# Optimization experiments

Hardware: AMD Instinct MI355X
Metric: run time of the kernel (lower is better)

## Reference

```python
import jax, jax.numpy as jnp
from jax import lax
import numpy as np

H = 64
NS = 20000
NR = 2000
T = 24
ALPHA = 0.5


def _p(key, *shape):
    return jax.random.normal(key, shape, dtype=jnp.float32) * 0.05


def setup_inputs() -> dict:
    key = jax.random.key(0)
    ks = jax.random.split(key, 40)
    inp = {
        "x_store": jax.random.normal(ks[0], (NS, T), dtype=jnp.float32),
        "x_region": jax.random.normal(ks[1], (NR, T), dtype=jnp.float32),
        "edge_ss": jax.random.randint(ks[2], (2, 640000), 0, NS),
        "edge_rs_src": jax.random.randint(ks[3], (160000,), 0, NR),
        "edge_rs_dst": jax.random.randint(ks[4], (160000,), 0, NS),
        "edge_sr_src": jax.random.randint(ks[5], (160000,), 0, NS),
        "edge_sr_dst": jax.random.randint(ks[6], (160000,), 0, NR),
        # LSTM pretransform params (torch gate order i,f,g,o)
        "Wih_s": _p(ks[7], 4 * H, 1), "Whh_s": _p(ks[8], 4 * H, H),
        "bih_s": _p(ks[9], 4 * H), "bhh_s": _p(ks[10], 4 * H),
        "Wih_r": _p(ks[11], 4 * H, 1), "Whh_r": _p(ks[12], 4 * H, H),
        "bih_r": _p(ks[13], 4 * H), "bhh_r": _p(ks[14], 4 * H),
        # DirSageConv (store-store)
        "W_s2d": _p(ks[15], H, H), "b_s2d": _p(ks[16], H),
        "W_d2s": _p(ks[17], H, H), "b_d2s": _p(ks[18], H),
        "W_self": _p(ks[19], H, H), "b_self": _p(ks[20], H),
        # SAGEConv region->store (lin_l w/ bias, lin_r no bias)
        "Wl_rs": _p(ks[21], H, H), "bl_rs": _p(ks[22], H), "Wr_rs": _p(ks[23], H, H),
        # SAGEConv store->region
        "Wl_sr": _p(ks[24], H, H), "bl_sr": _p(ks[25], H), "Wr_sr": _p(ks[26], H, H),
        # final linear
        "Wf": _p(ks[27], H, H), "bf": _p(ks[28], H),
    }
    return inp


def lstm_last(x, Wih, Whh, bih, bhh):
    # x: [N, T] scalar sequences (input_size=1). Returns last hidden state [N, H].
    N = x.shape[0]
    w_in = Wih[:, 0]  # [4H]
    b = bih + bhh

    def step(carry, xt):
        h, c = carry
        gates = xt[:, None] * w_in[None, :] + h @ Whh.T + b  # [N, 4H]
        i, f, g, o = jnp.split(gates, 4, axis=1)
        c = jax.nn.sigmoid(f) * c + jax.nn.sigmoid(i) * jnp.tanh(g)
        h = jax.nn.sigmoid(o) * jnp.tanh(c)
        return (h, c), None

    z = jnp.zeros((N, Whh.shape[1]), x.dtype)
    (h, _), _ = lax.scan(step, (z, z), x.T)
    return h


def mean_aggr(feats, dst_idx, num_dst):
    # mean of gathered edge messages per destination node (0 for isolated nodes)
    s = jax.ops.segment_sum(feats, dst_idx, num_segments=num_dst)
    cnt = jax.ops.segment_sum(jnp.ones(dst_idx.shape, feats.dtype), dst_idx, num_segments=num_dst)
    return s / jnp.maximum(cnt, 1.0)[:, None]


def reference(x_store, x_region, edge_ss, edge_rs_src, edge_rs_dst,
              edge_sr_src, edge_sr_dst,
              Wih_s, Whh_s, bih_s, bhh_s, Wih_r, Whh_r, bih_r, bhh_r,
              W_s2d, b_s2d, W_d2s, b_d2s, W_self, b_self,
              Wl_rs, bl_rs, Wr_rs, Wl_sr, bl_sr, Wr_sr, Wf, bf):
    # per-node-type LSTM pretransform -> [N, H]
    hs = lstm_last(x_store, Wih_s, Whh_s, bih_s, bhh_s)
    hr = lstm_last(x_region, Wih_r, Whh_r, bih_r, bhh_r)

    # DirSageConv on (store, link, store)
    src, dst = edge_ss[0], edge_ss[1]
    a_fwd = mean_aggr(hs[src], dst, NS) @ W_s2d.T + b_s2d   # src -> dst
    a_rev = mean_aggr(hs[dst], src, NS) @ W_d2s.T + b_d2s   # dst -> src
    dir_out = hs @ W_self.T + b_self + (1.0 - ALPHA) * a_fwd + ALPHA * a_rev

    # SAGEConv (region, influences, store)
    rs_out = mean_aggr(hr[edge_rs_src], edge_rs_dst, NS) @ Wl_rs.T + bl_rs + hs @ Wr_rs.T

    # SAGEConv (store, rev_influences, region)
    sr_out = mean_aggr(hs[edge_sr_src], edge_sr_dst, NR) @ Wl_sr.T + bl_sr + hr @ Wr_sr.T

    # HeteroConv aggr='mean' over edge types per dst node type
    store_h = (dir_out + rs_out) * 0.5
    region_h = sr_out

    # residual + relu
    store_h = jax.nn.relu(store_h + hs)
    region_h = jax.nn.relu(region_h + hr)  # computed as in torch, unused by output

    return store_h @ Wf.T + bf
```

## Files before the change

kernel.cpp:

```cpp
#include <hip/hip_runtime.h>
#include <hip/hip_bf16.h>

#define TT 24
#define NSTORE 20000
#define NREGION 2000
#define NE_SS 640000
#define NE_RS 160000
#define BN 32
#define SUBS 96
#define NGRP 8
#define CAPF 80
#define CAPS 32
#define POISON ((int)0xAAAAAAAAu)

typedef __attribute__((ext_vector_type(8))) short bf16x8;
typedef __attribute__((ext_vector_type(4))) float f32x4;

__device__ __forceinline__ float rcpf(float x) { return __builtin_amdgcn_rcpf(x); }
__device__ __forceinline__ float sigm(float x) { return rcpf(1.0f + __expf(-x)); }
__device__ __forceinline__ float tanh_(float x) { return fmaf(-2.0f, rcpf(1.0f + __expf(2.0f * x)), 1.0f); }

__device__ __forceinline__ short f2bs(float x) {
    __hip_bfloat16 h = __float2bfloat16(x);
    return *reinterpret_cast<short*>(&h);
}
__device__ __forceinline__ bf16x8 pack8(float4 a, float4 b) {
    bf16x8 r;
    r[0] = f2bs(a.x); r[1] = f2bs(a.y); r[2] = f2bs(a.z); r[3] = f2bs(a.w);
    r[4] = f2bs(b.x); r[5] = f2bs(b.y); r[6] = f2bs(b.z); r[7] = f2bs(b.w);
    return r;
}
__device__ __forceinline__ unsigned packbf2(float lo, float hi) {
    return ((unsigned)(unsigned short)f2bs(hi) << 16) | (unsigned)(unsigned short)f2bs(lo);
}
__device__ __forceinline__ float bf_lo(unsigned u) { return __uint_as_float(u << 16); }
__device__ __forceinline__ float bf_hi(unsigned u) { return __uint_as_float(u & 0xffff0000u); }

__device__ __forceinline__ f32x4 mfma16(bf16x8 a, bf16x8 b, f32x4 c) {
    return __builtin_amdgcn_mfma_f32_16x16x32_bf16(a, b, c, 0, 0, 0);
}

__global__ __launch_bounds__(256)
void lstm_fill(const float* __restrict__ xs, const float* __restrict__ WihS,
               const float* __restrict__ WhhS, const float* __restrict__ bihS,
               const float* __restrict__ bhhS,
               const float* __restrict__ xr, const float* __restrict__ WihR,
               const float* __restrict__ WhhR, const float* __restrict__ bihR,
               const float* __restrict__ bhhR,
               unsigned* __restrict__ hsOut, unsigned* __restrict__ hrOut,
               const int* __restrict__ ss_src, const int* __restrict__ ss_dst,
               const int* __restrict__ rs_src, const int* __restrict__ rs_dst,
               int* __restrict__ curF, int* __restrict__ curR, int* __restrict__ curS,
               int* __restrict__ eidF, int* __restrict__ eidR, int* __restrict__ eidS,
               int nBlocksStore, int nBlocksLstm)
{
    const int tid = threadIdx.x;

    if ((int)blockIdx.x >= nBlocksLstm) {
        const int fb = (int)blockIdx.x - nBlocksLstm;
        const int g = fb & (NGRP - 1);
        const int sub = fb / NGRP;
        const int lo = g * (NSTORE / NGRP), hi = lo + NSTORE / NGRP;
        const int stride = SUBS * 256;

        for (int t = sub * 256 + tid; t < NE_SS / 4; t += stride) {
            const int4 s4 = ((const int4*)ss_src)[t];
            const int4 d4 = ((const int4*)ss_dst)[t];
            const int ss[4] = {s4.x, s4.y, s4.z, s4.w};
            const int dd[4] = {d4.x, d4.y, d4.z, d4.w};
            #pragma unroll
            for (int e = 0; e < 4; ++e) {
                if (dd[e] >= lo && dd[e] < hi) {
                    int p = atomicAdd(&curF[dd[e]], 1) - POISON;
                    if (p < CAPF) eidF[dd[e] * CAPF + p] = ss[e];
                }
                if (ss[e] >= lo && ss[e] < hi) {
                    int p = atomicAdd(&curR[ss[e]], 1) - POISON;
                    if (p < CAPF) eidR[ss[e] * CAPF + p] = dd[e];
                }
            }
        }
        for (int t = sub * 256 + tid; t < NE_RS / 4; t += stride) {
            const int4 s4 = ((const int4*)rs_src)[t];
            const int4 d4 = ((const int4*)rs_dst)[t];
            const int ss[4] = {s4.x, s4.y, s4.z, s4.w};
            const int dd[4] = {d4.x, d4.y, d4.z, d4.w};
            #pragma unroll
            for (int e = 0; e < 4; ++e) {
                if (dd[e] >= lo && dd[e] < hi) {
                    int p = atomicAdd(&curS[dd[e]], 1) - POISON;
                    if (p < CAPS) eidS[dd[e] * CAPS + p] = ss[e];
                }
            }
        }
        return;
    }

    __shared__ unsigned hbU[2][32][36];
    __shared__ float xbuf[BN][25];

    const float *x, *Wih, *Whh, *bih, *bhh;
    unsigned* hout; int N, node0;
    if ((int)blockIdx.x < nBlocksStore) {
        x = xs; Wih = WihS; Whh = WhhS; bih = bihS; bhh = bhhS;
        hout = hsOut; N = NSTORE; node0 = blockIdx.x * BN;
    } else {
        x = xr; Wih = WihR; Whh = WhhR; bih = bihR; bhh = bhhR;
        hout = hrOut; N = NREGION; node0 = ((int)blockIdx.x - nBlocksStore) * BN;
    }

    const int w = tid >> 6, lane = tid & 63;
    const int l15 = lane & 15, q = lane >> 4;

    for (int i = tid; i < BN * TT; i += 256) {
        int n = i / TT, t = i - n * TT;
        int gn = node0 + n;
        xbuf[n][t] = (gn < N) ? x[gn * TT + t] : 0.0f;
    }

    bf16x8 Bf[4][2];
    #pragma unroll
    for (int g = 0; g < 4; ++g)
        #pragma unroll
        for (int kt = 0; kt < 2; ++kt) {
            const float* wrow = Whh + (g * 64 + (w << 4) + l15) * 64 + q * 8 + kt * 32;
            float4 v0 = *(const float4*)wrow;
            float4 v1 = *(const float4*)(wrow + 4);
            Bf[g][kt] = pack8(v0, v1);
        }

    float win[4], bsum[4];
    #pragma unroll
    for (int g = 0; g < 4; ++g) {
        int gi = g * 64 + (w << 4) + l15;
        win[g]  = Wih[gi];
        bsum[g] = bih[gi] + bhh[gi];
    }

    __syncthreads();

    float cc[2][4], hv[2][4];
    #pragma unroll
    for (int m = 0; m < 2; ++m)
        #pragma unroll
        for (int r = 0; r < 4; ++r) cc[m][r] = 0.0f;

    for (int t = 0; t < TT; ++t) {
        const int cur = t & 1, prev = cur ^ 1;

        bf16x8 Af[2][2];
        if (t > 0) {
            #pragma unroll
            for (int m = 0; m < 2; ++m)
                #pragma unroll
                for (int kt = 0; kt < 2; ++kt)
                    Af[m][kt] = *(const bf16x8*)&hbU[prev][l15 + 16 * m][(q << 2) + (kt << 4)];
        }

        f32x4 acc[4][2];
        float xv[2][4];
        #pragma unroll
        for (int m = 0; m < 2; ++m)
            #pragma unroll
            for (int r = 0; r < 4; ++r) xv[m][r] = xbuf[16 * m + q * 4 + r][t];
        #pragma unroll
        for (int g = 0; g < 4; ++g)
            #pragma unroll
            for (int m = 0; m < 2; ++m)
                #pragma unroll
                for (int r = 0; r < 4; ++r)
                    acc[g][m][r] = fmaf(xv[m][r], win[g], bsum[g]);

        if (t > 0) {
            #pragma unroll
            for (int g = 0; g < 4; ++g)
                #pragma unroll
                for (int m = 0; m < 2; ++m) {
                    acc[g][m] = mfma16(Af[m][0], Bf[g][0], acc[g][m]);
                    acc[g][m] = mfma16(Af[m][1], Bf[g][1], acc[g][m]);
                }
        }

        #pragma unroll
        for (int m = 0; m < 2; ++m)
            #pragma unroll
            for (int r = 0; r < 4; ++r) {
                float ig = sigm(acc[0][m][r]);
                float fg = sigm(acc[1][m][r]);
                float gg = tanh_(acc[2][m][r]);
                float og = sigm(acc[3][m][r]);
                float cn = fmaf(fg, cc[m][r], ig * gg);
                cc[m][r] = cn;
                hv[m][r] = og * tanh_(cn);
            }

        #pragma unroll
        for (int m = 0; m < 2; ++m)
            #pragma unroll
            for (int r = 0; r < 4; ++r) {
                float other = __shfl_xor(hv[m][r], 1);
                if ((l15 & 1) == 0)
                    hbU[cur][16 * m + 4 * q + r][(w << 3) + (l15 >> 1)] = packbf2(hv[m][r], other);
            }
        __syncthreads();
    }

    for (int i = tid; i < 32 * 32; i += 256) {
        int n = i >> 5, kp = i & 31;
        int gn = node0 + n;
        if (gn < N) hout[gn * 32 + kp] = hbU[1][n][kp];
    }
}

__global__ __launch_bounds__(256)
void gather_means(const unsigned* __restrict__ hsU, const unsigned* __restrict__ hrU,
                  const int* __restrict__ curF, const int* __restrict__ curR,
                  const int* __restrict__ curS,
                  const int* __restrict__ eidF, const int* __restrict__ eidR,
                  const int* __restrict__ eidS,
                  unsigned* __restrict__ xcatU)
{
    const int id = blockIdx.x * 4 + (threadIdx.x >> 6);
    const int lane = threadIdx.x & 63;
    const int sec = id / NSTORE;
    const int n   = id - sec * NSTORE;
    const int o8 = lane >> 3, l7 = lane & 7;

    unsigned* row = xcatU + (size_t)n * 128;

    if (sec == 0 && lane < 32) row[lane] = hsU[n * 32 + lane];

    const unsigned* feat = (sec == 2) ? hrU : hsU;
    const int* seg; int cnt, cap;
    if (sec == 0)      { seg = eidF + n * CAPF; cnt = curF[n] - POISON; cap = CAPF; }
    else if (sec == 1) { seg = eidR + n * CAPF; cnt = curR[n] - POISON; cap = CAPF; }
    else               { seg = eidS + n * CAPS; cnt = curS[n] - POISON; cap = CAPS; }
    int e = cnt < cap ? cnt : cap;

    float a[8];
    #pragma unroll
    for (int k = 0; k < 8; ++k) a[k] = 0.0f;

    for (int i = 0; i < e; i += 16) {
        int i0 = i + o8;
        if (i0 < e) {
            uint4 u = *(const uint4*)&feat[seg[i0] * 32 + 4 * l7];
            a[0] += bf_lo(u.x); a[1] += bf_hi(u.x);
            a[2] += bf_lo(u.y); a[3] += bf_hi(u.y);
            a[4] += bf_lo(u.z); a[5] += bf_hi(u.z);
            a[6] += bf_lo(u.w); a[7] += bf_hi(u.w);
        }
        int i1 = i + 8 + o8;
        if (i1 < e) {
            uint4 u = *(const uint4*)&feat[seg[i1] * 32 + 4 * l7];
            a[0] += bf_lo(u.x); a[1] += bf_hi(u.x);
            a[2] += bf_lo(u.y); a[3] += bf_hi(u.y);
            a[4] += bf_lo(u.z); a[5] += bf_hi(u.z);
            a[6] += bf_lo(u.w); a[7] += bf_hi(u.w);
        }
    }
    #pragma unroll
    for (int k = 0; k < 8; ++k) {
        a[k] += __shfl_xor(a[k], 8);
        a[k] += __shfl_xor(a[k], 16);
        a[k] += __shfl_xor(a[k], 32);
    }
    float c = rcpf(fmaxf((float)cnt, 1.0f));
    if (lane < 8) {
        uint4 o;
        o.x = packbf2(a[0] * c, a[1] * c);
        o.y = packbf2(a[2] * c, a[3] * c);
        o.z = packbf2(a[4] * c, a[5] * c);
        o.w = packbf2(a[6] * c, a[7] * c);
        *(uint4*)&row[(sec + 1) * 32 + 4 * l7] = o;
    }
}

__global__ __launch_bounds__(256, 2)
void combine_mm(const unsigned* __restrict__ xcatU,
                const float* __restrict__ Ws2d, const float* __restrict__ bs2d,
                const float* __restrict__ Wd2s, const float* __restrict__ bd2s,
                const float* __restrict__ Wself, const float* __restrict__ bself,
                const float* __restrict__ Wlrs, const float* __restrict__ blrs,
                const float* __restrict__ Wrrs,
                const float* __restrict__ Wfm, const float* __restrict__ bfv,
                float* __restrict__ out)
{
    __shared__ float Xs[64][68];
    __shared__ float Ps[64][64];
    __shared__ float Us[64][68];
    __shared__ float Wfs[64][68];
    __shared__ float biasc[64];

    const int tid = threadIdx.x;
    const int node0 = blockIdx.x * 64;

    for (int i = tid; i < 4096; i += 256) {
        int jp = i >> 6, j = i & 63;
        Wfs[j][jp] = Wfm[i];
    }
    if (tid < 64)
        biasc[tid] = bself[tid] + 0.5f * bs2d[tid] + 0.5f * bd2s[tid] + blrs[tid];

    const int jg = tid & 15, ng = tid >> 4;
    const int j0 = jg * 4, n0 = ng * 4;

    float acc[4][4];
    #pragma unroll
    for (int dn = 0; dn < 4; ++dn)
        #pragma unroll
        for (int dj = 0; dj < 4; ++dj) acc[dn][dj] = 0.0f;

    const int sj = tid >> 2, skb = tid & 3;

    for (int ci = 0; ci < 4; ++ci) {
        const int c = (ci + 1) & 3;
        __syncthreads();

        {
            int n = tid >> 2;
            int gn = node0 + n; if (gn > NSTORE - 1) gn = NSTORE - 1;
            const unsigned* src = xcatU + (size_t)gn * 128 + c * 32 + (tid & 3) * 8;
            uint4 u0 = *(const uint4*)src;
            uint4 u1 = *(const uint4*)(src + 4);
            unsigned uu[8] = {u0.x, u0.y, u0.z, u0.w, u1.x, u1.y, u1.z, u1.w};
            int k0 = (tid & 3) * 16;
            #pragma unroll
            for (int e = 0; e < 8; ++e) {
                Xs[k0 + 2 * e][n]     = bf_lo(uu[e]);
                Xs[k0 + 2 * e + 1][n] = bf_hi(uu[e]);
            }
        }
        {
            const float* W1; float scale;
            if (c == 0)      { W1 = Wself; scale = 1.0f; }
            else if (c == 1) { W1 = Ws2d;  scale = 0.5f; }
            else if (c == 2) { W1 = Wd2s;  scale = 0.5f; }
            else             { W1 = Wlrs;  scale = 1.0f; }
            #pragma unroll
            for (int qq = 0; qq < 4; ++qq) {
                int k0 = skb * 16 + qq * 4;
                float4 v = *(const float4*)(W1 + sj * 64 + k0);
                if (c == 0) {
                    float4 v2 = *(const float4*)(Wrrs + sj * 64 + k0);
                    v.x += v2.x; v.y += v2.y; v.z += v2.z; v.w += v2.w;
                } else {
                    v.x *= scale; v.y *= scale; v.z *= scale; v.w *= scale;
                }
                Ps[k0][sj] = v.x; Ps[k0 + 1][sj] = v.y;
                Ps[k0 + 2][sj] = v.z; Ps[k0 + 3][sj] = v.w;
            }
        }
        __syncthreads();

        #pragma unroll 4
        for (int k = 0; k < 64; ++k) {
            float4 wv = *(const float4*)&Ps[k][j0];
            float4 xv = *(const float4*)&Xs[k][n0];
            float x4[4] = {xv.x, xv.y, xv.z, xv.w};
            float w4[4] = {wv.x, wv.y, wv.z, wv.w};
            #pragma unroll
            for (int dn = 0; dn < 4; ++dn)
                #pragma unroll
                for (int dj = 0; dj < 4; ++dj)
                    acc[dn][dj] = fmaf(x4[dn], w4[dj], acc[dn][dj]);
        }
    }

    #pragma unroll
    for (int dn = 0; dn < 4; ++dn)
        #pragma unroll
        for (int dj = 0; dj < 4; ++dj) {
            float h = Xs[j0 + dj][n0 + dn];
            float u = fmaxf(fmaf(0.5f, acc[dn][dj] + biasc[j0 + dj], h), 0.0f);
            Us[j0 + dj][n0 + dn] = u;
        }
    __syncthreads();

    float o[4][4];
    #pragma unroll
    for (int dn = 0; dn < 4; ++dn)
        #pragma unroll
        for (int dj = 0; dj < 4; ++dj) o[dn][dj] = 0.0f;

    #pragma unroll 4
    for (int k = 0; k < 64; ++k) {
        float4 wv = *(const float4*)&Wfs[k][j0];
        float4 uv = *(const float4*)&Us[k][n0];
        float u4[4] = {uv.x, uv.y, uv.z, uv.w};
        float w4[4] = {wv.x, wv.y, wv.z, wv.w};
        #pragma unroll
        for (int dn = 0; dn < 4; ++dn)
            #pragma unroll
            for (int dj = 0; dj < 4; ++dj)
                o[dn][dj] = fmaf(u4[dn], w4[dj], o[dn][dj]);
    }

    float4 bfe = *(const float4*)(bfv + j0);
    #pragma unroll
    for (int dn = 0; dn < 4; ++dn) {
        int gn = node0 + n0 + dn;
        if (gn < NSTORE) {
            float4 v = make_float4(o[dn][0] + bfe.x, o[dn][1] + bfe.y,
                                   o[dn][2] + bfe.z, o[dn][3] + bfe.w);
            *(float4*)&out[gn * 64 + j0] = v;
        }
    }
}

extern "C" void kernel_launch(void* const* d_in, const int* in_sizes, int n_in,
                              void* d_out, int out_size, void* d_ws, size_t ws_size,
                              hipStream_t stream)
{
    const float* xs     = (const float*)d_in[0];
    const float* xr     = (const float*)d_in[1];
    const int*   e_ss   = (const int*)d_in[2];
    const int*   rs_src = (const int*)d_in[3];
    const int*   rs_dst = (const int*)d_in[4];
    const float* WihS = (const float*)d_in[7];
    const float* WhhS = (const float*)d_in[8];
    const float* bihS = (const float*)d_in[9];
    const float* bhhS = (const float*)d_in[10];
    const float* WihR = (const float*)d_in[11];
    const float* WhhR = (const float*)d_in[12];
    const float* bihR = (const float*)d_in[13];
    const float* bhhR = (const float*)d_in[14];
    const float* Ws2d = (const float*)d_in[15];
    const float* bs2d = (const float*)d_in[16];
    const float* Wd2s = (const float*)d_in[17];
    const float* bd2s = (const float*)d_in[18];
    const float* Wself = (const float*)d_in[19];
    const float* bself = (const float*)d_in[20];
    const float* Wlrs = (const float*)d_in[21];
    const float* blrs = (const float*)d_in[22];
    const float* Wrrs = (const float*)d_in[23];
    const float* Wfm = (const float*)d_in[27];
    const float* bfv = (const float*)d_in[28];

    const int* ss_src = e_ss;
    const int* ss_dst = e_ss + NE_SS;

    unsigned* hsU   = (unsigned*)d_ws;
    unsigned* hrU   = hsU + 640000;
    unsigned* xcatU = hrU + 64000;
    int*      ib    = (int*)(xcatU + 2560000);
    int* curF = ib;
    int* curR = ib + 20000;
    int* curS = ib + 40000;
    int* eidF = ib + 60000;
    int* eidR = eidF + NSTORE * CAPF;
    int* eidS = eidR + NSTORE * CAPF;

    const int storeBlocks  = (NSTORE + BN - 1) / BN;
    const int regionBlocks = (NREGION + BN - 1) / BN;
    const int lstmBlocks   = storeBlocks + regionBlocks;
    const int fillBlocks   = NGRP * SUBS;

    lstm_fill<<<lstmBlocks + fillBlocks, 256, 0, stream>>>(
        xs, WihS, WhhS, bihS, bhhS, xr, WihR, WhhR, bihR, bhhR,
        hsU, hrU, ss_src, ss_dst, rs_src, rs_dst,
        curF, curR, curS, eidF, eidR, eidS,
        storeBlocks, lstmBlocks);

    gather_means<<<3 * NSTORE / 4, 256, 0, stream>>>(hsU, hrU,
                                                     curF, curR, curS,
                                                     eidF, eidR, eidS, xcatU);

    combine_mm<<<(NSTORE + 63) / 64, 256, 0, stream>>>(xcatU,
                                                       Ws2d, bs2d, Wd2s, bd2s,
                                                       Wself, bself, Wlrs, blrs, Wrrs,
                                                       Wfm, bfv, (float*)d_out);
}
```

Baseline: 274.8 us.

## Split fused LSTM/edge-bucketing kernel into separate sequential launches

Breaks the combined kernel, where LSTM blocks and edge-bucketing blocks ran side by side in one grid, into two launches: an edge fill kernel followed by an LSTM-only kernel. Each kernel gets its own register and occupancy profile, so the fill work is no longer constrained by the LSTM kernel's resource use. The cost is that the two phases no longer overlap on the GPU and there is an extra launch. The index loads also switch to nontemporal loads.

```diff
diff --git a/kernel.cpp b/kernel.cpp
--- a/kernel.cpp
+++ b/kernel.cpp
@@ -15,6 +15,7 @@
 
 typedef __attribute__((ext_vector_type(8))) short bf16x8;
 typedef __attribute__((ext_vector_type(4))) float f32x4;
+typedef __attribute__((ext_vector_type(4))) int int4v;
 
 __device__ __forceinline__ float rcpf(float x) { return __builtin_amdgcn_rcpf(x); }
 __device__ __forceinline__ float sigm(float x) { return rcpf(1.0f + __expf(-x)); }
@@ -41,60 +42,59 @@
 }
 
 __global__ __launch_bounds__(256)
-void lstm_fill(const float* __restrict__ xs, const float* __restrict__ WihS,
+void fill_seg(const int* __restrict__ ss_src, const int* __restrict__ ss_dst,
+              const int* __restrict__ rs_src, const int* __restrict__ rs_dst,
+              int* __restrict__ curF, int* __restrict__ curR, int* __restrict__ curS,
+              int* __restrict__ eidF, int* __restrict__ eidR, int* __restrict__ eidS)
+{
+    const int tid = threadIdx.x;
+    const int fb = (int)blockIdx.x;
+    const int g = fb & (NGRP - 1);
+    const int sub = fb / NGRP;
+    const int lo = g * (NSTORE / NGRP), hi = lo + NSTORE / NGRP;
+    const int stride = SUBS * 256;
+
+    for (int t = sub * 256 + tid; t < NE_SS / 4; t += stride) {
+        const int4v s4 = __builtin_nontemporal_load(&((const int4v*)ss_src)[t]);
+        const int4v d4 = __builtin_nontemporal_load(&((const int4v*)ss_dst)[t]);
+        #pragma unroll
+        for (int e = 0; e < 4; ++e) {
+            const int se = s4[e], de = d4[e];
+            if (de >= lo && de < hi) {
+                int p = atomicAdd(&curF[de], 1) - POISON;
+                if (p < CAPF) eidF[de * CAPF + p] = se;
+            }
+            if (se >= lo && se < hi) {
+                int p = atomicAdd(&curR[se], 1) - POISON;
+                if (p < CAPF) eidR[se * CAPF + p] = de;
+            }
+        }
+    }
+    for (int t = sub * 256 + tid; t < NE_RS / 4; t += stride) {
+        const int4v s4 = __builtin_nontemporal_load(&((const int4v*)rs_src)[t]);
+        const int4v d4 = __builtin_nontemporal_load(&((const int4v*)rs_dst)[t]);
+        #pragma unroll
+        for (int e = 0; e < 4; ++e) {
+            const int se = s4[e], de = d4[e];
+            if (de >= lo && de < hi) {
+                int p = atomicAdd(&curS[de], 1) - POISON;
+                if (p < CAPS) eidS[de * CAPS + p] = se;
+            }
+        }
+    }
+}
+
+__global__ __launch_bounds__(256)
+void lstm_only(const float* __restrict__ xs, const float* __restrict__ WihS,
                const float* __restrict__ WhhS, const float* __restrict__ bihS,
                const float* __restrict__ bhhS,
                const float* __restrict__ xr, const float* __restrict__ WihR,
                const float* __restrict__ WhhR, const float* __restrict__ bihR,
                const float* __restrict__ bhhR,
                unsigned* __restrict__ hsOut, unsigned* __restrict__ hrOut,
-               const int* __restrict__ ss_src, const int* __restrict__ ss_dst,
-               const int* __restrict__ rs_src, const int* __restrict__ rs_dst,
-               int* __restrict__ curF, int* __restrict__ curR, int* __restrict__ curS,
-               int* __restrict__ eidF, int* __restrict__ eidR, int* __restrict__ eidS,
-               int nBlocksStore, int nBlocksLstm)
+               int nBlocksStore)
 {
     const int tid = threadIdx.x;
-
-    if ((int)blockIdx.x >= nBlocksLstm) {
-        const int fb = (int)blockIdx.x - nBlocksLstm;
-        const int g = fb & (NGRP - 1);
-        const int sub = fb / NGRP;
-        const int lo = g * (NSTORE / NGRP), hi = lo + NSTORE / NGRP;
-        const int stride = SUBS * 256;
-
-        for (int t = sub * 256 + tid; t < NE_SS / 4; t += stride) {
-            const int4 s4 = ((const int4*)ss_src)[t];
-            const int4 d4 = ((const int4*)ss_dst)[t];
-            const int ss[4] = {s4.x, s4.y, s4.z, s4.w};
-            const int dd[4] = {d4.x, d4.y, d4.z, d4.w};
-            #pragma unroll
-            for (int e = 0; e < 4; ++e) {
-                if (dd[e] >= lo && dd[e] < hi) {
-                    int p = atomicAdd(&curF[dd[e]], 1) - POISON;
-                    if (p < CAPF) eidF[dd[e] * CAPF + p] = ss[e];
-                }
-                if (ss[e] >= lo && ss[e] < hi) {
-                    int p = atomicAdd(&curR[ss[e]], 1) - POISON;
-                    if (p < CAPF) eidR[ss[e] * CAPF + p] = dd[e];
-                }
-            }
-        }
-        for (int t = sub * 256 + tid; t < NE_RS / 4; t += stride) {
-            const int4 s4 = ((const int4*)rs_src)[t];
-            const int4 d4 = ((const int4*)rs_dst)[t];
-            const int ss[4] = {s4.x, s4.y, s4.z, s4.w};
-            const int dd[4] = {d4.x, d4.y, d4.z, d4.w};
-            #pragma unroll
-            for (int e = 0; e < 4; ++e) {
-                if (dd[e] >= lo && dd[e] < hi) {
-                    int p = atomicAdd(&curS[dd[e]], 1) - POISON;
-                    if (p < CAPS) eidS[dd[e] * CAPS + p] = ss[e];
-                }
-            }
-        }
-        return;
-    }
 
     __shared__ unsigned hbU[2][32][36];
     __shared__ float xbuf[BN][25];
@@ -456,11 +456,12 @@
     const int lstmBlocks   = storeBlocks + regionBlocks;
     const int fillBlocks   = NGRP * SUBS;
 
-    lstm_fill<<<lstmBlocks + fillBlocks, 256, 0, stream>>>(
+    fill_seg<<<fillBlocks, 256, 0, stream>>>(ss_src, ss_dst, rs_src, rs_dst,
+                                             curF, curR, curS, eidF, eidR, eidS);
+
+    lstm_only<<<lstmBlocks, 256, 0, stream>>>(
         xs, WihS, WhhS, bihS, bhhS, xr, WihR, WhhR, bihR, bhhR,
-        hsU, hrU, ss_src, ss_dst, rs_src, rs_dst,
-        curF, curR, curS, eidF, eidR, eidS,
-        storeBlocks, lstmBlocks);
+        hsU, hrU, storeBlocks);
 
     gather_means<<<3 * NSTORE / 4, 256, 0, stream>>>(hsU, hrU,
                                                      curF, curR, curS,
```

Result: slower. 312.7 us (+13.8%).
